# Optimization experiments

Hardware: AMD Instinct MI355X
Metric: run time of the kernel (lower is better)

The kernel has to match this reference:

```python
import jax, jax.numpy as jnp
import numpy as np

N_HEADS = 16  # cfg.n_heads
ROPE_BASE = 10000.0


def _rope_sin_cos(T, head_dim, dtype):
    # standard NeoX-style rotary tables, shape (T, head_dim)
    inv_freq = 1.0 / (ROPE_BASE ** (jnp.arange(0, head_dim, 2, dtype=jnp.float32) / head_dim))
    freqs = jnp.arange(T, dtype=jnp.float32)[:, None] * inv_freq[None, :]  # (T, hd/2)
    emb = jnp.concatenate([freqs, freqs], axis=-1)                          # (T, hd)
    return jnp.sin(emb).astype(dtype), jnp.cos(emb).astype(dtype)


def _rotate_half(x):
    x1, x2 = jnp.split(x, 2, axis=-1)
    return jnp.concatenate([-x2, x1], axis=-1)


def setup_inputs() -> dict:
    key = jax.random.key(0)
    kx, kq, kp, kl = jax.random.split(key, 4)
    B, T, D = 4, 2048, 2048
    x = jax.random.normal(kx, (B, T, D), dtype=jnp.float32)
    # torch Linear weights: (out_features, in_features), no bias
    Wqkv = jax.random.normal(kq, (3 * D, D), dtype=jnp.float32) * (D ** -0.5)
    Wproj = jax.random.normal(kp, (D, D), dtype=jnp.float32) * (D ** -0.5)
    # padding at the end: valid lengths in [T//2, T]
    lengths = jax.random.randint(kl, (B,), T // 2, T + 1)
    attention_mask = (jnp.arange(T)[None, :] < lengths[:, None]).astype(jnp.int32)
    return {"x": x, "Wqkv": Wqkv, "Wproj": Wproj, "attention_mask": attention_mask}


def reference(x, Wqkv, Wproj, attention_mask):
    B, T, D = x.shape
    H = N_HEADS
    hd = D // H
    qkv = (x @ Wqkv.T).reshape(B, T, 3, H, hd)            # (B,T,3,H,hd)
    q, k, v = (jnp.moveaxis(qkv[:, :, i], 1, 2) for i in range(3))  # each (B,H,T,hd)
    sin, cos = _rope_sin_cos(T, hd, x.dtype)              # (T,hd), broadcast over B,H
    q = q * cos + _rotate_half(q) * sin
    k = k * cos + _rotate_half(k) * sin
    scale = 1.0 / jnp.sqrt(jnp.asarray(hd, x.dtype))
    scores = jnp.einsum("bhqd,bhkd->bhqk", q, k) * scale  # (B,H,T,T)
    causal = jnp.triu(jnp.ones((T, T), dtype=bool), k=1)[None, None]       # (1,1,T,T)
    pad = (attention_mask == 0)[:, None, None, :]                           # (B,1,1,T)
    bias = jnp.where(causal | pad, -jnp.inf, 0.0).astype(x.dtype)
    attn = jax.nn.softmax(scores + bias, axis=-1)
    out = jnp.einsum("bhqk,bhkd->bhqd", attn, v)          # (B,H,T,hd)
    out = jnp.moveaxis(out, 1, 2).reshape(B, T, D)
    return out @ Wproj.T
```

## Files before the change

### kernel.cpp

```cpp
#include <hip/hip_runtime.h>
#include <math.h>

#define B_SZ 4
#define T_SEQ 2048
#define D_MODEL 2048
#define NH 16
#define HD 128

typedef unsigned short u16;
typedef unsigned int u32;
typedef __attribute__((ext_vector_type(8))) short short8;
typedef __attribute__((ext_vector_type(4))) float f32x4;

__device__ __forceinline__ float bf2f(u16 u) {
    return __uint_as_float(((u32)u) << 16);
}
__device__ __forceinline__ u16 f2bf(float f) {
    u32 x = __float_as_uint(f);
    return (u16)((x + 0x7fffu + ((x >> 16) & 1u)) >> 16);
}

__device__ __forceinline__ void gload_lds16(const u16* g, u16* lds) {
    __builtin_amdgcn_global_load_lds(
        (const __attribute__((address_space(1))) u32*)(const void*)g,
        (__attribute__((address_space(3))) u32*)(void*)lds, 16, 0, 0);
}

__global__ __launch_bounds__(256) void cast_kernel(const float* __restrict__ in,
                                                   u16* __restrict__ out, int n4)
{
    int idx = blockIdx.x * 256 + threadIdx.x;
    if (idx < n4) {
        float4 x = ((const float4*)in)[idx];
        ushort4 u;
        u.x = f2bf(x.x); u.y = f2bf(x.y); u.z = f2bf(x.z); u.w = f2bf(x.w);
        ((ushort4*)out)[idx] = u;
    }
}

#define TSZ 16384
#define MFMA_B16 __builtin_amdgcn_mfma_f32_16x16x32_bf16

template <int MODE>
__global__ __launch_bounds__(512, 2) void gemm256(
    const u16* __restrict__ A, const u16* __restrict__ W,
    float* __restrict__ C,
    u16* __restrict__ qb, u16* __restrict__ kb, u16* __restrict__ vb,
    int M, int N, int K)
{
    extern __shared__ u16 smem[];

    const int tid = threadIdx.x;
    const int nbx = N >> 8;
    const int nwg = gridDim.x;
    const int orig = blockIdx.x;
    const int wgid = (orig & 7) * (nwg >> 3) + (orig >> 3);
    const int bx = wgid % nbx, by = wgid / nbx;
    const int n0 = bx << 8, m0 = by << 8;

    const int w = tid >> 6, L = tid & 63;
    const int wm = w >> 2, wn = w & 3;
    const int lr = L & 15;
    const int lqb = (L >> 4) << 4;
    const int xorv = (lr & 7) << 4;
    const int cb0 = lqb ^ xorv;
    const int cb1 = (64 + lqb) ^ xorv;

    const u16* Ag = A + (size_t)m0 * K;
    const u16* Wg = W + (size_t)n0 * K;

    const int srow = tid >> 3;
    const int scb = ((tid << 4) & 127) ^ ((srow & 7) << 4);
    const size_t goff = (size_t)srow * K + (scb >> 1);
    const int loff = tid << 3;

    const int NT = K >> 6;

    f32x4 acc[8][4];
#pragma unroll
    for (int i = 0; i < 8; ++i)
#pragma unroll
        for (int j = 0; j < 4; ++j) acc[i][j] = (f32x4){0.f, 0.f, 0.f, 0.f};

#define ST_A(tt, c) gload_lds16(Ag + (size_t)((c) * 64) * K + (size_t)(tt) * 64 + goff, \
                                smem + ((tt) & 1) * TSZ + (c) * 4096 + loff)
#define ST_B(tt, c) gload_lds16(Wg + (size_t)((c) * 64) * K + (size_t)(tt) * 64 + goff, \
                                smem + 2 * TSZ + ((tt) & 1) * TSZ + (c) * 4096 + loff)

    ST_A(0, 0); ST_A(0, 2); ST_B(0, 0); ST_B(0, 1); ST_B(0, 2); ST_B(0, 3);
    ST_A(0, 1); ST_A(0, 3);
    ST_A(1, 0); ST_A(1, 2); ST_B(1, 0); ST_B(1, 1); ST_B(1, 2); ST_B(1, 3);
    asm volatile("s_waitcnt vmcnt(6)" ::: "memory");
    __builtin_amdgcn_s_barrier();

    for (int t = 0; t < NT; ++t) {
        const char* pA = (const char*)(smem + (t & 1) * TSZ) + (wm * 128 + lr) * 128;
        const char* pB = (const char*)(smem + 2 * TSZ + (t & 1) * TSZ) + (wn * 64 + lr) * 128;
        short8 alo[4][2], ahi[4][2], blo[2][2], bhi[2][2];

#pragma unroll
        for (int f = 0; f < 4; ++f) {
            alo[f][0] = *(const short8*)(pA + f * 2048 + cb0);
            alo[f][1] = *(const short8*)(pA + f * 2048 + cb1);
        }
#pragma unroll
        for (int g = 0; g < 2; ++g) {
            blo[g][0] = *(const short8*)(pB + g * 2048 + cb0);
            blo[g][1] = *(const short8*)(pB + g * 2048 + cb1);
        }
        if (t + 1 < NT) { ST_A(t + 1, 1); ST_A(t + 1, 3); }
        asm volatile("s_waitcnt lgkmcnt(8)" ::: "memory");
        __builtin_amdgcn_s_barrier();
        asm volatile("s_waitcnt lgkmcnt(0)" ::: "memory");
        __builtin_amdgcn_sched_barrier(0);
        __builtin_amdgcn_s_setprio(1);
#pragma unroll
        for (int f = 0; f < 4; ++f)
#pragma unroll
            for (int g = 0; g < 2; ++g) {
                acc[f][g] = MFMA_B16(alo[f][0], blo[g][0], acc[f][g], 0, 0, 0);
                acc[f][g] = MFMA_B16(alo[f][1], blo[g][1], acc[f][g], 0, 0, 0);
            }
        __builtin_amdgcn_s_setprio(0);
        __builtin_amdgcn_s_barrier();

#pragma unroll
        for (int g = 0; g < 2; ++g) {
            bhi[g][0] = *(const short8*)(pB + 4096 + g * 2048 + cb0);
            bhi[g][1] = *(const short8*)(pB + 4096 + g * 2048 + cb1);
        }
        if (t + 2 < NT) { ST_A(t + 2, 0); ST_A(t + 2, 2); }
        __builtin_amdgcn_s_barrier();
        asm volatile("s_waitcnt lgkmcnt(0)" ::: "memory");
        __builtin_amdgcn_sched_barrier(0);
        __builtin_amdgcn_s_setprio(1);
#pragma unroll
        for (int f = 0; f < 4; ++f)
#pragma unroll
            for (int g = 0; g < 2; ++g) {
                acc[f][2 + g] = MFMA_B16(alo[f][0], bhi[g][0], acc[f][2 + g], 0, 0, 0);
                acc[f][2 + g] = MFMA_B16(alo[f][1], bhi[g][1], acc[f][2 + g], 0, 0, 0);
            }
        __builtin_amdgcn_s_setprio(0);
        __builtin_amdgcn_s_barrier();

#pragma unroll
        for (int f = 0; f < 4; ++f) {
            ahi[f][0] = *(const short8*)(pA + 8192 + f * 2048 + cb0);
            ahi[f][1] = *(const short8*)(pA + 8192 + f * 2048 + cb1);
        }
        if (t + 2 < NT) { ST_B(t + 2, 0); ST_B(t + 2, 1); }
        __builtin_amdgcn_s_barrier();
        asm volatile("s_waitcnt lgkmcnt(0)" ::: "memory");
        __builtin_amdgcn_sched_barrier(0);
        __builtin_amdgcn_s_setprio(1);
#pragma unroll
        for (int f = 0; f < 4; ++f)
#pragma unroll
            for (int g = 0; g < 2; ++g) {
                acc[4 + f][g] = MFMA_B16(ahi[f][0], blo[g][0], acc[4 + f][g], 0, 0, 0);
                acc[4 + f][g] = MFMA_B16(ahi[f][1], blo[g][1], acc[4 + f][g], 0, 0, 0);
            }
        __builtin_amdgcn_s_setprio(0);
        __builtin_amdgcn_s_barrier();

        if (t + 2 < NT) { ST_B(t + 2, 2); ST_B(t + 2, 3); }
        if (t < NT - 2)
            asm volatile("s_waitcnt vmcnt(6)" ::: "memory");
        else
            asm volatile("s_waitcnt vmcnt(0)" ::: "memory");
        __builtin_amdgcn_s_barrier();
        __builtin_amdgcn_s_setprio(1);
#pragma unroll
        for (int f = 0; f < 4; ++f)
#pragma unroll
            for (int g = 0; g < 2; ++g) {
                acc[4 + f][2 + g] = MFMA_B16(ahi[f][0], bhi[g][0], acc[4 + f][2 + g], 0, 0, 0);
                acc[4 + f][2 + g] = MFMA_B16(ahi[f][1], bhi[g][1], acc[4 + f][2 + g], 0, 0, 0);
            }
        __builtin_amdgcn_s_setprio(0);
        __builtin_amdgcn_s_barrier();
    }
#undef ST_A
#undef ST_B

    const int lq4 = (L >> 4) << 2;

    if (MODE == 0) {
#pragma unroll
        for (int f = 0; f < 8; ++f) {
            const int m = m0 + wm * 128 + (f >> 2) * 64 + (f & 3) * 16 + lq4;
#pragma unroll
            for (int g = 0; g < 4; ++g) {
                const int n = n0 + wn * 64 + (g >> 1) * 32 + (g & 1) * 16 + lr;
#pragma unroll
                for (int r = 0; r < 4; ++r)
                    C[(size_t)(m + r) * N + n] = acc[f][g][r];
            }
        }
    } else {
        const int s = n0 >> 11;
        const int b_ = m0 >> 11;
        const int t0 = m0 & (T_SEQ - 1);
        if (s == 2) {
            u16* Ts = smem;
#pragma unroll
            for (int f = 0; f < 8; ++f) {
                const int tl = wm * 128 + (f >> 2) * 64 + (f & 3) * 16 + lq4;
#pragma unroll
                for (int g = 0; g < 4; ++g) {
                    const int c = wn * 64 + (g >> 1) * 32 + (g & 1) * 16 + lr;
                    char* rowp = (char*)Ts + c * 512;
#pragma unroll
                    for (int r = 0; r < 4; ++r)
                        *(u16*)(rowp + (((tl + r) * 2) ^ ((c & 7) << 4))) =
                            f2bf(acc[f][g][r]);
                }
            }
            __syncthreads();
            const int h0 = (n0 & 2047) >> 7;
            const int tcb = (tid & 31) << 4;
#pragma unroll
            for (int pass = 0; pass < 16; ++pass) {
                const int c = pass * 16 + (tid >> 5);
                short8 vv = *(const short8*)((const char*)Ts + c * 512 +
                                             (tcb ^ ((c & 7) << 4)));
                const int hh = c >> 7, d = c & 127;
                *(short8*)(vb + ((size_t)(b_ * NH + h0 + hh) * HD + d) * T_SEQ +
                           t0 + (tcb >> 1)) = vv;
            }
        } else {
            u16* p = (s == 0) ? qb : kb;
            const int nb = n0 & 2047;
#pragma unroll
            for (int f = 0; f < 8; ++f) {
                const int tl = t0 + wm * 128 + (f >> 2) * 64 + (f & 3) * 16 + lq4;
#pragma unroll
                for (int g = 0; g < 4; ++g) {
                    const int nn = nb + wn * 64 + (g >> 1) * 32 + (g & 1) * 16 + lr;
                    const int hh = nn >> 7, d = nn & 127;
                    u16* pb = p + ((size_t)(b_ * NH + hh) * T_SEQ + tl) * HD + d;
#pragma unroll
                    for (int r = 0; r < 4; ++r)
                        pb[(size_t)r * HD] = f2bf(acc[f][g][r]);
                }
            }
        }
    }
}

__global__ __launch_bounds__(128) void rope_kernel(u16* __restrict__ qb,
                                                   u16* __restrict__ kb)
{
    const int bht = blockIdx.x;
    const int t = bht & (T_SEQ - 1);
    const int bh = bht >> 11;
    const int tid = threadIdx.x;
    const int i = tid & 63;
    u16* buf = (tid < 64) ? qb : kb;
    const size_t base = ((size_t)bh * T_SEQ + t) * HD;

    const float inv = expf(-(2.f * (float)i / 128.f) * 9.210340371976184f);
    const float ang = (float)t * inv;
    const float s = sinf(ang);
    const float c = cosf(ang);

    const float x1 = bf2f(buf[base + i]);
    const float x2 = bf2f(buf[base + i + 64]);
    buf[base + i]      = f2bf(x1 * c - x2 * s);
    buf[base + i + 64] = f2bf(x2 * c + x1 * s);
}

__device__ __forceinline__ void stage_k_512(const u16* g, u16* lds, int tid) {
#pragma unroll
    for (int c = 0; c < 2; ++c) {
        const int row = c * 32 + (tid >> 4);
        const int cb = ((tid & 15) * 16) ^ ((row & 7) << 4);
        gload_lds16(g + (size_t)row * HD + (cb >> 1), lds + c * 4096 + tid * 8);
    }
}
__device__ __forceinline__ void stage_v_512(const u16* g, u16* lds, int tid) {
#pragma unroll
    for (int c = 0; c < 2; ++c) {
        const int row = c * 64 + (tid >> 3);
        const int cb = ((tid & 7) * 16) ^ ((row & 7) << 4);
        gload_lds16(g + (size_t)row * T_SEQ + (cb >> 1), lds + c * 4096 + tid * 8);
    }
}

__global__ __launch_bounds__(512, 2) void attn_kernel(
    const u16* __restrict__ q, const u16* __restrict__ k,
    const u16* __restrict__ v, const int* __restrict__ mask,
    u16* __restrict__ o)
{
    extern __shared__ u16 smem[];
    u16* Kb = smem;
    u16* Vb = smem + 16384;

    const int tid = threadIdx.x;
    const int orig = blockIdx.x;
    const int xcd = orig & 7;
    const int slot = orig >> 3;
    const int bh = xcd + ((slot >> 4) << 3);
    const int qi = 15 - (slot & 15);
    const int b = bh >> 4;
    const int q0 = qi * 128;
    const int w = tid >> 6, L = tid & 63;
    const int lr = L & 15;
    const int lqB = (L >> 4) * 16;
    const int xk = (lr & 7) << 4;
    const float scale = 0.08838834764831845f;
    const float NEG = -1e30f;

    char* PsW = (char*)smem + 65536 + w * 2048;

    const u16* qg = q + (size_t)bh * T_SEQ * HD;
    const u16* kg = k + (size_t)bh * T_SEQ * HD;
    const u16* vg = v + (size_t)bh * HD * T_SEQ;
    const int* mrow = mask + b * T_SEQ;

#pragma unroll
    for (int c = 0; c < 4; ++c) {
        const int row = c * 32 + (tid >> 4);
        const int cb = ((tid & 15) * 16) ^ ((row & 7) << 4);
        gload_lds16(qg + (size_t)(q0 + row) * HD + (cb >> 1),
                    smem + c * 4096 + tid * 8);
    }
    int4 m4 = ((const int4*)mrow)[tid];
    int part = m4.x + m4.y + m4.z + m4.w;
#pragma unroll
    for (int off = 32; off >= 1; off >>= 1) part += __shfl_xor(part, off);
    int* lred = (int*)((char*)smem + 65536);
    if (L == 0) lred[w] = part;
    __syncthreads();
    int len = 0;
#pragma unroll
    for (int i = 0; i < 8; ++i) len += lred[i];

    short8 qa[4];
    {
        const char* Qc = (const char*)smem;
        const int row = w * 16 + lr;
#pragma unroll
        for (int kc = 0; kc < 4; ++kc)
            qa[kc] = *(const short8*)(Qc + row * 256 + ((kc * 64 + lqB) ^ xk));
    }
    __syncthreads();

    const int ntk = (len + 63) >> 6;
    const int lim0 = 2 * qi + 1;
    const int lim = (lim0 < ntk - 1) ? lim0 : (ntk - 1);

    stage_k_512(kg, Kb, tid);
    stage_v_512(vg, Vb, tid);

    f32x4 on[8];
#pragma unroll
    for (int nd = 0; nd < 8; ++nd) on[nd] = (f32x4){0.f, 0.f, 0.f, 0.f};
    float l_r[4] = {0.f, 0.f, 0.f, 0.f};
    const int wrow0 = q0 + w * 16;
    const int row_base = wrow0 + (L >> 4) * 4;

    for (int kt = 0; kt <= lim; ++kt) {
        const int kv0 = kt * 64;
        const int cur = kt & 1;
        if (kt < lim) {
            stage_k_512(kg + (size_t)(kv0 + 64) * HD, Kb + (cur ^ 1) * 8192, tid);
            stage_v_512(vg + (kv0 + 64), Vb + (cur ^ 1) * 8192, tid);
            asm volatile("s_waitcnt vmcnt(4)" ::: "memory");
        } else {
            asm volatile("s_waitcnt vmcnt(0)" ::: "memory");
        }
        __builtin_amdgcn_s_barrier();

        const bool active = (kv0 <= wrow0 + 15);
        if (active) {
            const char* Kc = (const char*)(Kb + cur * 8192);
            const char* Vc = (const char*)(Vb + cur * 8192);

            f32x4 sacc[4];
#pragma unroll
            for (int nt = 0; nt < 4; ++nt) {
                const char* rp = Kc + (nt * 16 + lr) * 256;
                short8 bb[4];
#pragma unroll
                for (int kc = 0; kc < 4; ++kc)
                    bb[kc] = *(const short8*)(rp + ((kc * 64 + lqB) ^ xk));
                sacc[nt] = (f32x4){0.f, 0.f, 0.f, 0.f};
                __builtin_amdgcn_s_setprio(1);
#pragma unroll
                for (int kc = 0; kc < 4; ++kc)
                    sacc[nt] = MFMA_B16(qa[kc], bb[kc], sacc[nt], 0, 0, 0);
                __builtin_amdgcn_s_setprio(0);
            }

            const bool diag = (kv0 + 63 > wrow0);
#pragma unroll
            for (int nt = 0; nt < 4; ++nt) {
                const int col = kv0 + nt * 16 + lr;
                const float bias = (col < len) ? 0.f : NEG;
#pragma unroll
                for (int r = 0; r < 4; ++r) {
                    float s = sacc[nt][r] * scale + bias;
                    if (diag && col > row_base + r) s = NEG;
                    const float p = __expf(s);
                    l_r[r] += p;
                    const int pr = (L >> 4) * 4 + r;
                    *(u16*)(PsW + pr * 128 +
                            (((nt * 16 + lr) * 2) ^ ((pr & 7) << 4))) = f2bf(p);
                }
            }

            short8 pa0 = *(const short8*)(PsW + lr * 128 + (lqB ^ xk));
            short8 pa1 = *(const short8*)(PsW + lr * 128 + ((64 + lqB) ^ xk));
            __builtin_amdgcn_s_setprio(1);
#pragma unroll
            for (int nd = 0; nd < 8; ++nd) {
                const char* vp = Vc + (nd * 16 + lr) * 128;
                short8 vb0 = *(const short8*)(vp + (lqB ^ xk));
                short8 vb1 = *(const short8*)(vp + ((64 + lqB) ^ xk));
                on[nd] = MFMA_B16(pa0, vb0, on[nd], 0, 0, 0);
                on[nd] = MFMA_B16(pa1, vb1, on[nd], 0, 0, 0);
            }
            __builtin_amdgcn_s_setprio(0);
        }
        __builtin_amdgcn_s_barrier();
    }

#pragma unroll
    for (int off = 1; off < 16; off <<= 1)
#pragma unroll
        for (int r = 0; r < 4; ++r)
            l_r[r] += __shfl_xor(l_r[r], off);

    const int h = bh & 15;
#pragma unroll
    for (int r = 0; r < 4; ++r) {
        const float inv = 1.f / l_r[r];
        const int t = row_base + r;
        u16* op = o + ((size_t)(b * T_SEQ + t)) * D_MODEL + h * HD + lr;
#pragma unroll
        for (int nd = 0; nd < 8; ++nd)
            op[nd * 16] = f2bf(on[nd][r] * inv);
    }
}

extern "C" void kernel_launch(void* const* d_in, const int* in_sizes, int n_in,
                              void* d_out, int out_size, void* d_ws, size_t ws_size,
                              hipStream_t stream)
{
    const float* x     = (const float*)d_in[0];
    const float* Wqkv  = (const float*)d_in[1];
    const float* Wproj = (const float*)d_in[2];
    const int*   mask  = (const int*)d_in[3];
    float* out = (float*)d_out;

    const size_t E = (size_t)B_SZ * T_SEQ * D_MODEL;
    u16* xb     = (u16*)d_ws;
    u16* wqkvb  = xb + E;
    u16* wprojb = wqkvb + (size_t)3 * D_MODEL * D_MODEL;
    u16* qb     = wprojb + (size_t)D_MODEL * D_MODEL;
    u16* kb     = qb + E;
    u16* vb     = kb + E;
    u16* ob     = vb + E;

    const int M = B_SZ * T_SEQ;

    cast_kernel<<<dim3((int)(E / 4 / 256)), 256, 0, stream>>>(x, xb, (int)(E / 4));
    cast_kernel<<<dim3(3 * D_MODEL * D_MODEL / 4 / 256), 256, 0, stream>>>(
        Wqkv, wqkvb, 3 * D_MODEL * D_MODEL / 4);
    cast_kernel<<<dim3(D_MODEL * D_MODEL / 4 / 256), 256, 0, stream>>>(
        Wproj, wprojb, D_MODEL * D_MODEL / 4);

    gemm256<1><<<dim3((3 * D_MODEL / 256) * (M / 256)), 512, 131072, stream>>>(
        xb, wqkvb, nullptr, qb, kb, vb, M, 3 * D_MODEL, D_MODEL);

    rope_kernel<<<dim3(B_SZ * NH * T_SEQ), 128, 0, stream>>>(qb, kb);

    attn_kernel<<<dim3(16 * 64), 512, 81920, stream>>>(qb, kb, vb, mask, ob);

    gemm256<0><<<dim3((D_MODEL / 256) * (M / 256)), 512, 131072, stream>>>(
        ob, wprojb, out, nullptr, nullptr, nullptr, M, D_MODEL, D_MODEL);
}
```

Baseline: 587.3 us.

## Double attention query tile per block and merge three cast kernels into one

The attention kernel now handles 256 query rows per workgroup, 32 per wave as two 16-row sub-tiles. Each K/V tile staged in LDS is therefore reused by twice as many MFMAs, and the grid is halved. The three fp32-to-bf16 cast launches are also merged into one kernel that selects its source buffer by index. The cost is more registers for the accumulators, more LDS (96KB), fewer workgroups, and coarser causal work balance, which may reduce occupancy.

New measurement: 577.4 us. About the same (-1.7%).

```diff
diff --git a/kernel.cpp b/kernel.cpp
--- a/kernel.cpp
+++ b/kernel.cpp
@@ -26,16 +26,24 @@
         (__attribute__((address_space(3))) u32*)(void*)lds, 16, 0, 0);
 }
 
-__global__ __launch_bounds__(256) void cast_kernel(const float* __restrict__ in,
-                                                   u16* __restrict__ out, int n4)
+__global__ __launch_bounds__(256) void cast_all(
+    const float* __restrict__ x, const float* __restrict__ wq,
+    const float* __restrict__ wp,
+    u16* __restrict__ xb, u16* __restrict__ wqb, u16* __restrict__ wpb)
 {
+    const int NX = (B_SZ * T_SEQ * D_MODEL) / 4;
+    const int NQ = (3 * D_MODEL * D_MODEL) / 4;
     int idx = blockIdx.x * 256 + threadIdx.x;
-    if (idx < n4) {
-        float4 x = ((const float4*)in)[idx];
-        ushort4 u;
-        u.x = f2bf(x.x); u.y = f2bf(x.y); u.z = f2bf(x.z); u.w = f2bf(x.w);
-        ((ushort4*)out)[idx] = u;
-    }
+    const float* in;
+    u16* out;
+    int off;
+    if (idx < NX)           { in = x;  out = xb;  off = idx; }
+    else if (idx < NX + NQ) { in = wq; out = wqb; off = idx - NX; }
+    else                    { in = wp; out = wpb; off = idx - NX - NQ; }
+    float4 v = ((const float4*)in)[off];
+    ushort4 u;
+    u.x = f2bf(v.x); u.y = f2bf(v.y); u.z = f2bf(v.z); u.w = f2bf(v.w);
+    ((ushort4*)out)[off] = u;
 }
 
 #define TSZ 16384
@@ -301,10 +309,10 @@
     const int orig = blockIdx.x;
     const int xcd = orig & 7;
     const int slot = orig >> 3;
-    const int bh = xcd + ((slot >> 4) << 3);
-    const int qi = 15 - (slot & 15);
+    const int bh = xcd + ((slot >> 3) << 3);
+    const int qi = 7 - (slot & 7);
     const int b = bh >> 4;
-    const int q0 = qi * 128;
+    const int q0 = qi * 256;
     const int w = tid >> 6, L = tid & 63;
     const int lr = L & 15;
     const int lqB = (L >> 4) * 16;
@@ -312,7 +320,7 @@
     const float scale = 0.08838834764831845f;
     const float NEG = -1e30f;
 
-    char* PsW = (char*)smem + 65536 + w * 2048;
+    char* PsW = (char*)smem + 65536 + w * 4096;
 
     const u16* qg = q + (size_t)bh * T_SEQ * HD;
     const u16* kg = k + (size_t)bh * T_SEQ * HD;
@@ -320,7 +328,7 @@
     const int* mrow = mask + b * T_SEQ;
 
 #pragma unroll
-    for (int c = 0; c < 4; ++c) {
+    for (int c = 0; c < 8; ++c) {
         const int row = c * 32 + (tid >> 4);
         const int cb = ((tid & 15) * 16) ^ ((row & 7) << 4);
         gload_lds16(qg + (size_t)(q0 + row) * HD + (cb >> 1),
@@ -337,29 +345,34 @@
 #pragma unroll
     for (int i = 0; i < 8; ++i) len += lred[i];
 
-    short8 qa[4];
+    short8 qa[2][4];
     {
         const char* Qc = (const char*)smem;
-        const int row = w * 16 + lr;
-#pragma unroll
-        for (int kc = 0; kc < 4; ++kc)
-            qa[kc] = *(const short8*)(Qc + row * 256 + ((kc * 64 + lqB) ^ xk));
+#pragma unroll
+        for (int rt = 0; rt < 2; ++rt) {
+            const int row = w * 32 + rt * 16 + lr;
+#pragma unroll
+            for (int kc = 0; kc < 4; ++kc)
+                qa[rt][kc] =
+                    *(const short8*)(Qc + row * 256 + ((kc * 64 + lqB) ^ xk));
+        }
     }
     __syncthreads();
 
     const int ntk = (len + 63) >> 6;
-    const int lim0 = 2 * qi + 1;
+    const int lim0 = 4 * qi + 3;
     const int lim = (lim0 < ntk - 1) ? lim0 : (ntk - 1);
 
     stage_k_512(kg, Kb, tid);
     stage_v_512(vg, Vb, tid);
 
-    f32x4 on[8];
-#pragma unroll
-    for (int nd = 0; nd < 8; ++nd) on[nd] = (f32x4){0.f, 0.f, 0.f, 0.f};
-    float l_r[4] = {0.f, 0.f, 0.f, 0.f};
-    const int wrow0 = q0 + w * 16;
-    const int row_base = wrow0 + (L >> 4) * 4;
+    f32x4 on[2][8];
+#pragma unroll
+    for (int rt = 0; rt < 2; ++rt)
+#pragma unroll
+        for (int nd = 0; nd < 8; ++nd) on[rt][nd] = (f32x4){0.f, 0.f, 0.f, 0.f};
+    float l_r[2][4] = {{0.f, 0.f, 0.f, 0.f}, {0.f, 0.f, 0.f, 0.f}};
+    const int wrow0 = q0 + w * 32;
 
     for (int kt = 0; kt <= lim; ++kt) {
         const int kv0 = kt * 64;
@@ -373,12 +386,12 @@
         }
         __builtin_amdgcn_s_barrier();
 
-        const bool active = (kv0 <= wrow0 + 15);
+        const bool active = (kv0 <= wrow0 + 31);
         if (active) {
             const char* Kc = (const char*)(Kb + cur * 8192);
             const char* Vc = (const char*)(Vb + cur * 8192);
 
-            f32x4 sacc[4];
+            f32x4 s0[4], s1[4];
 #pragma unroll
             for (int nt = 0; nt < 4; ++nt) {
                 const char* rp = Kc + (nt * 16 + lr) * 256;
@@ -386,41 +399,57 @@
 #pragma unroll
                 for (int kc = 0; kc < 4; ++kc)
                     bb[kc] = *(const short8*)(rp + ((kc * 64 + lqB) ^ xk));
-                sacc[nt] = (f32x4){0.f, 0.f, 0.f, 0.f};
+                s0[nt] = (f32x4){0.f, 0.f, 0.f, 0.f};
+                s1[nt] = (f32x4){0.f, 0.f, 0.f, 0.f};
                 __builtin_amdgcn_s_setprio(1);
 #pragma unroll
-                for (int kc = 0; kc < 4; ++kc)
-                    sacc[nt] = MFMA_B16(qa[kc], bb[kc], sacc[nt], 0, 0, 0);
+                for (int kc = 0; kc < 4; ++kc) {
+                    s0[nt] = MFMA_B16(qa[0][kc], bb[kc], s0[nt], 0, 0, 0);
+                    s1[nt] = MFMA_B16(qa[1][kc], bb[kc], s1[nt], 0, 0, 0);
+                }
                 __builtin_amdgcn_s_setprio(0);
             }
 
-            const bool diag = (kv0 + 63 > wrow0);
-#pragma unroll
-            for (int nt = 0; nt < 4; ++nt) {
-                const int col = kv0 + nt * 16 + lr;
-                const float bias = (col < len) ? 0.f : NEG;
-#pragma unroll
-                for (int r = 0; r < 4; ++r) {
-                    float s = sacc[nt][r] * scale + bias;
-                    if (diag && col > row_base + r) s = NEG;
-                    const float p = __expf(s);
-                    l_r[r] += p;
-                    const int pr = (L >> 4) * 4 + r;
-                    *(u16*)(PsW + pr * 128 +
-                            (((nt * 16 + lr) * 2) ^ ((pr & 7) << 4))) = f2bf(p);
+#pragma unroll
+            for (int rt = 0; rt < 2; ++rt) {
+                const int rb = wrow0 + rt * 16 + (L >> 4) * 4;
+                const bool diag = (kv0 + 63 > wrow0 + rt * 16);
+#pragma unroll
+                for (int nt = 0; nt < 4; ++nt) {
+                    const int col = kv0 + nt * 16 + lr;
+                    const float bias = (col < len) ? 0.f : NEG;
+#pragma unroll
+                    for (int r = 0; r < 4; ++r) {
+                        float s = (rt ? s1[nt][r] : s0[nt][r]) * scale + bias;
+                        if (diag && col > rb + r) s = NEG;
+                        const float p = __expf(s);
+                        l_r[rt][r] += p;
+                        const int pr = rt * 16 + (L >> 4) * 4 + r;
+                        *(u16*)(PsW + pr * 128 +
+                                (((nt * 16 + lr) * 2) ^ ((pr & 7) << 4))) =
+                            f2bf(p);
+                    }
                 }
             }
 
-            short8 pa0 = *(const short8*)(PsW + lr * 128 + (lqB ^ xk));
-            short8 pa1 = *(const short8*)(PsW + lr * 128 + ((64 + lqB) ^ xk));
+            short8 pa[2][2];
+#pragma unroll
+            for (int rt = 0; rt < 2; ++rt) {
+                pa[rt][0] = *(const short8*)(PsW + (rt * 16 + lr) * 128 +
+                                             (lqB ^ xk));
+                pa[rt][1] = *(const short8*)(PsW + (rt * 16 + lr) * 128 +
+                                             ((64 + lqB) ^ xk));
+            }
             __builtin_amdgcn_s_setprio(1);
 #pragma unroll
             for (int nd = 0; nd < 8; ++nd) {
                 const char* vp = Vc + (nd * 16 + lr) * 128;
                 short8 vb0 = *(const short8*)(vp + (lqB ^ xk));
                 short8 vb1 = *(const short8*)(vp + ((64 + lqB) ^ xk));
-                on[nd] = MFMA_B16(pa0, vb0, on[nd], 0, 0, 0);
-                on[nd] = MFMA_B16(pa1, vb1, on[nd], 0, 0, 0);
+                on[0][nd] = MFMA_B16(pa[0][0], vb0, on[0][nd], 0, 0, 0);
+                on[0][nd] = MFMA_B16(pa[0][1], vb1, on[0][nd], 0, 0, 0);
+                on[1][nd] = MFMA_B16(pa[1][0], vb0, on[1][nd], 0, 0, 0);
+                on[1][nd] = MFMA_B16(pa[1][1], vb1, on[1][nd], 0, 0, 0);
             }
             __builtin_amdgcn_s_setprio(0);
         }
@@ -430,18 +459,24 @@
 #pragma unroll
     for (int off = 1; off < 16; off <<= 1)
 #pragma unroll
-        for (int r = 0; r < 4; ++r)
-            l_r[r] += __shfl_xor(l_r[r], off);
+        for (int rt = 0; rt < 2; ++rt)
+#pragma unroll
+            for (int r = 0; r < 4; ++r)
+                l_r[rt][r] += __shfl_xor(l_r[rt][r], off);
 
     const int h = bh & 15;
 #pragma unroll
-    for (int r = 0; r < 4; ++r) {
-        const float inv = 1.f / l_r[r];
-        const int t = row_base + r;
-        u16* op = o + ((size_t)(b * T_SEQ + t)) * D_MODEL + h * HD + lr;
-#pragma unroll
-        for (int nd = 0; nd < 8; ++nd)
-            op[nd * 16] = f2bf(on[nd][r] * inv);
+    for (int rt = 0; rt < 2; ++rt) {
+        const int rb = wrow0 + rt * 16 + (L >> 4) * 4;
+#pragma unroll
+        for (int r = 0; r < 4; ++r) {
+            const float inv = 1.f / l_r[rt][r];
+            const int t = rb + r;
+            u16* op = o + ((size_t)(b * T_SEQ + t)) * D_MODEL + h * HD + lr;
+#pragma unroll
+            for (int nd = 0; nd < 8; ++nd)
+                op[nd * 16] = f2bf(on[rt][nd][r] * inv);
+        }
     }
 }
 
@@ -465,19 +500,18 @@
     u16* ob     = vb + E;
 
     const int M = B_SZ * T_SEQ;
-
-    cast_kernel<<<dim3((int)(E / 4 / 256)), 256, 0, stream>>>(x, xb, (int)(E / 4));
-    cast_kernel<<<dim3(3 * D_MODEL * D_MODEL / 4 / 256), 256, 0, stream>>>(
-        Wqkv, wqkvb, 3 * D_MODEL * D_MODEL / 4);
-    cast_kernel<<<dim3(D_MODEL * D_MODEL / 4 / 256), 256, 0, stream>>>(
-        Wproj, wprojb, D_MODEL * D_MODEL / 4);
+    const int NCAST = (int)(E / 4) + 3 * D_MODEL * D_MODEL / 4 +
+                      D_MODEL * D_MODEL / 4;
+
+    cast_all<<<dim3(NCAST / 256), 256, 0, stream>>>(x, Wqkv, Wproj, xb, wqkvb,
+                                                    wprojb);
 
     gemm256<1><<<dim3((3 * D_MODEL / 256) * (M / 256)), 512, 131072, stream>>>(
         xb, wqkvb, nullptr, qb, kb, vb, M, 3 * D_MODEL, D_MODEL);
 
     rope_kernel<<<dim3(B_SZ * NH * T_SEQ), 128, 0, stream>>>(qb, kb);
 
-    attn_kernel<<<dim3(16 * 64), 512, 81920, stream>>>(qb, kb, vb, mask, ob);
+    attn_kernel<<<dim3(8 * 64), 512, 98304, stream>>>(qb, kb, vb, mask, ob);
 
     gemm256<0><<<dim3((D_MODEL / 256) * (M / 256)), 512, 131072, stream>>>(
         ob, wprojb, out, nullptr, nullptr, nullptr, M, D_MODEL, D_MODEL);
```
